# Performance work log

Measured on AMD Instinct MI355X. Metric: run time of the kernel, lower is better.

## Reference

```python
import jax, jax.numpy as jnp
import numpy as np

N = 102400      # total nodes across batch of graphs
E = 1638400     # edges (before self-loops)
G = 256         # number of graphs
F_IN = 64       # node_feat_dim
H = 4           # heads (conv1)
C = 32          # hidden per head
CLIN = 5
NEG_SLOPE = 0.2


def setup_inputs() -> dict:
    key = jax.random.key(0)
    ks = jax.random.split(key, 16)
    s = 0.1
    x = jax.random.normal(ks[0], (N, F_IN), jnp.float32)
    edge_index = jax.random.randint(ks[1], (2, E), 0, N, dtype=jnp.int32)
    batch = (jnp.arange(N, dtype=jnp.int32) * G) // N  # sorted graph ids, 400 nodes each
    clinical = jax.random.normal(ks[2], (G, CLIN), jnp.float32)
    W1 = jax.random.normal(ks[3], (F_IN, H * C), jnp.float32) * s
    a_src1 = jax.random.normal(ks[4], (H, C), jnp.float32) * s
    a_dst1 = jax.random.normal(ks[5], (H, C), jnp.float32) * s
    b1 = jnp.zeros((H * C,), jnp.float32)
    # GATConv 2: 128 -> 32, 1 head, no concat (mean over heads = identity for 1 head)
    W2 = jax.random.normal(ks[6], (H * C, C), jnp.float32) * s
    a_src2 = jax.random.normal(ks[7], (1, C), jnp.float32) * s
    a_dst2 = jax.random.normal(ks[8], (1, C), jnp.float32) * s
    b2 = jnp.zeros((C,), jnp.float32)
    # Classifier: Linear(37,16) -> ELU -> Linear(16,1)
    Wc1 = jax.random.normal(ks[9], (C + CLIN, 16), jnp.float32) * s
    bc1 = jnp.zeros((16,), jnp.float32)
    Wc2 = jax.random.normal(ks[10], (16, 1), jnp.float32) * s
    bc2 = jnp.zeros((1,), jnp.float32)
    return dict(x=x, edge_index=edge_index, batch=batch, clinical=clinical,
                W1=W1, a_src1=a_src1, a_dst1=a_dst1, b1=b1,
                W2=W2, a_src2=a_src2, a_dst2=a_dst2, b2=b2,
                Wc1=Wc1, bc1=bc1, Wc2=Wc2, bc2=bc2)


def _gat(x, W, a_src, a_dst, b, src, dst, heads, concat):
    n = x.shape[0]
    h = (x @ W).reshape(n, heads, -1)                 # [N, H, C]
    al_src = jnp.einsum('nhc,hc->nh', h, a_src)       # [N, H]
    al_dst = jnp.einsum('nhc,hc->nh', h, a_dst)
    e = jax.nn.leaky_relu(al_src[src] + al_dst[dst], NEG_SLOPE)  # [E, H]
    # segment softmax over incoming edges of each destination node
    m = jax.ops.segment_max(e, dst, num_segments=n)
    ex = jnp.exp(e - m[dst])
    den = jax.ops.segment_sum(ex, dst, num_segments=n)
    alpha = ex / den[dst]                             # [E, H]
    msg = h[src] * alpha[:, :, None]                  # [E, H, C]
    out = jax.ops.segment_sum(msg, dst, num_segments=n)
    out = out.reshape(n, -1) if concat else out.mean(axis=1)
    return out + b


def reference(x, edge_index, batch, clinical,
              W1, a_src1, a_dst1, b1, W2, a_src2, a_dst2, b2,
              Wc1, bc1, Wc2, bc2):
    n = x.shape[0]
    loop = jnp.arange(n, dtype=edge_index.dtype)
    src = jnp.concatenate([edge_index[0], loop])      # PyG add_self_loops=True
    dst = jnp.concatenate([edge_index[1], loop])
    h = _gat(x, W1, a_src1, a_dst1, b1, src, dst, H, True)   # [N, 128]
    h = jax.nn.elu(h)
    h = _gat(h, W2, a_src2, a_dst2, b2, src, dst, 1, False)  # [N, 32]
    h = jax.nn.elu(h)
    # global mean pool per graph
    sums = jax.ops.segment_sum(h, batch, num_segments=G)
    cnt = jax.ops.segment_sum(jnp.ones((n,), h.dtype), batch, num_segments=G)
    pooled = sums / cnt[:, None]                      # [G, 32]
    fused = jnp.concatenate([pooled, clinical.reshape(-1, CLIN)], axis=1)  # [G, 37]
    z = jax.nn.elu(fused @ Wc1 + bc1)
    return z @ Wc2 + bc2                              # [G, 1]
```

## Files before the change

kernel.cpp:

```cpp
#include <hip/hip_runtime.h>
#include <math.h>

#define N_NODES 102400
#define N_EDGES 1638400
#define G_GRAPHS 256
#define NODES_PER_G 400
#define CAPB 7168
#define F_IN  64
#define H1    4
#define C1    32
#define F_MID 128
#define C2    32
#define CLIN  5
#define NEG   0.2f

__device__ __forceinline__ float lrelu(float x) { return x > 0.f ? x : NEG * x; }
__device__ __forceinline__ float elu(float x)   { return x > 0.f ? x : expm1f(x); }

__device__ __forceinline__ unsigned short f2bf(float f) {
    unsigned u = __float_as_uint(f);
    u = (u + 0x7fffu + ((u >> 16) & 1u)) >> 16;
    return (unsigned short)u;
}
__device__ __forceinline__ float bfLO(unsigned p) { return __uint_as_float(p << 16); }
__device__ __forceinline__ float bfHI(unsigned p) { return __uint_as_float(p & 0xffff0000u); }
__device__ __forceinline__ float4 bf2f4(uint2 p) {
    return make_float4(__uint_as_float(p.x << 16), __uint_as_float(p.x & 0xffff0000u),
                       __uint_as_float(p.y << 16), __uint_as_float(p.y & 0xffff0000u));
}

__global__ __launch_bounds__(256) void bin_k(const int* __restrict__ ei,
                                             int* __restrict__ gcnt,
                                             unsigned* __restrict__ binned) {
    __shared__ int hist[256];
    __shared__ int off[256];
    int t = threadIdx.x;
    hist[t] = 0;
    __syncthreads();
    int i0 = blockIdx.x * 4096;
#pragma unroll
    for (int j = 0; j < 16; ++j) {
        int d = ei[N_EDGES + i0 + j * 256 + t];
        atomicAdd(&hist[d / NODES_PER_G], 1);
    }
    __syncthreads();
    off[t] = atomicAdd(&gcnt[t], hist[t]);
    hist[t] = 0;
    __syncthreads();
#pragma unroll
    for (int j = 0; j < 16; ++j) {
        int idx = i0 + j * 256 + t;
        int s = ei[idx];
        int d = ei[N_EDGES + idx];
        int g = d / NODES_PER_G;
        int dl = d - g * NODES_PER_G;
        int slot = atomicAdd(&hist[g], 1);
        binned[(size_t)g * CAPB + off[g] + slot] = (unsigned)s | ((unsigned)dl << 17);
    }
}

__global__ __launch_bounds__(512) void build_k(
    const int* __restrict__ gcnt, unsigned* __restrict__ binned,
    int* __restrict__ row_ptr, int* __restrict__ row_end)
{
    __shared__ unsigned edg[CAPB];
    __shared__ int coll[CAPB];
    __shared__ int hist[512];
    __shared__ int cur[NODES_PER_G];
    int g = blockIdx.x, t = threadIdx.x;
    int ne = gcnt[g];
    size_t base = (size_t)g * CAPB;
    for (int i = t; i < ne; i += 512) edg[i] = binned[base + i];
    hist[t] = 0;
    __syncthreads();
    for (int i = t; i < ne; i += 512) atomicAdd(&hist[edg[i] >> 17], 1);
    __syncthreads();
    int v = hist[t];
    for (int off = 1; off < 512; off <<= 1) {
        int tmp = (t >= off) ? hist[t - off] : 0;
        __syncthreads();
        hist[t] += tmp;
        __syncthreads();
    }
    int excl = hist[t] - v;
    if (t < NODES_PER_G) {
        cur[t] = excl;
        row_ptr[g * NODES_PER_G + t] = (int)base + excl;
    }
    __syncthreads();
    for (int i = t; i < ne; i += 512) {
        unsigned e = edg[i];
        int pos = atomicAdd(&cur[e >> 17], 1);
        coll[pos] = (int)(e & 0x1FFFFu);
    }
    __syncthreads();
    if (t < NODES_PER_G) row_end[g * NODES_PER_G + t] = (int)base + cur[t];
    for (int i = t; i < ne; i += 512) binned[base + i] = (unsigned)coll[i];
}

__global__ __launch_bounds__(256) void ht_k(
    const float* __restrict__ x, const float* __restrict__ W1,
    const float* __restrict__ a_src1, const float* __restrict__ a_dst1,
    unsigned short* __restrict__ hth, float* __restrict__ al1)
{
    __shared__ float xs[32][65];
    __shared__ float W1s[64 * 160];
    int t = threadIdx.x;
    int n0 = blockIdx.x * 32;
#pragma unroll
    for (int j = 0; j < 8; ++j) {
        int idx = t + 256 * j;
        xs[idx >> 6][idx & 63] = x[(size_t)n0 * F_IN + idx];
    }
#pragma unroll
    for (int j = 0; j < 8; ++j) {
        int q = t + 256 * j;
        int k = q >> 5, c0 = (q & 31) * 4;
        float4 v = ((const float4*)W1)[q];
        *(float4*)&W1s[k * 160 + (c0 >> 4) * 20 + (c0 & 15)] = v;
    }
    __syncthreads();
    int n = t >> 3, cg = t & 7;
    float acc[16];
#pragma unroll
    for (int j = 0; j < 16; ++j) acc[j] = 0.f;
    const float* wp = &W1s[cg * 20];
#pragma unroll 4
    for (int k = 0; k < F_IN; ++k) {
        float a = xs[n][k];
        const float* wr = wp + k * 160;
#pragma unroll
        for (int j = 0; j < 4; ++j) {
            float4 w = *(const float4*)(wr + 4 * j);
            acc[4 * j + 0] += a * w.x;
            acc[4 * j + 1] += a * w.y;
            acc[4 * j + 2] += a * w.z;
            acc[4 * j + 3] += a * w.w;
        }
    }
    int head = cg >> 1, hoff = (cg & 1) * 16;
    const float* asp = a_src1 + head * 32 + hoff;
    const float* adp = a_dst1 + head * 32 + hoff;
    float ps = 0.f, pd = 0.f;
#pragma unroll
    for (int j = 0; j < 16; ++j) { ps += acc[j] * asp[j]; pd += acc[j] * adp[j]; }
    ps += __shfl_xor(ps, 1);
    pd += __shfl_xor(pd, 1);
    if ((cg & 1) == 0) {
        al1[(size_t)(n0 + n) * 8 + head]     = ps;
        al1[(size_t)(n0 + n) * 8 + 4 + head] = pd;
    }
    unsigned u[8];
#pragma unroll
    for (int j = 0; j < 8; ++j)
        u[j] = ((unsigned)f2bf(acc[2 * j + 1]) << 16) | (unsigned)f2bf(acc[2 * j]);
    uint4* hp = (uint4*)(hth + ((size_t)(n0 + n) * F_MID + cg * 16));
    hp[0] = make_uint4(u[0], u[1], u[2], u[3]);
    hp[1] = make_uint4(u[4], u[5], u[6], u[7]);
}

__global__ __launch_bounds__(256, 8) void agg1_k(
    const int* __restrict__ row_ptr, const int* __restrict__ row_end,
    const unsigned* __restrict__ col, const unsigned short* __restrict__ hth,
    const float* __restrict__ al1, const float* __restrict__ b1,
    float* __restrict__ h1)
{
    int t = threadIdx.x;
    int wv = t >> 6, lane = t & 63, h = lane >> 4;
    int d = blockIdx.x * 4 + wv;
    const unsigned* hv = (const unsigned*)hth;

    float adv = al1[d * 8 + 4 + h];
    float w = __expf(lrelu(al1[d * 8 + h] + adv));
    unsigned p = hv[(size_t)d * 64 + lane];
    float a0 = w * bfLO(p), a1 = w * bfHI(p);
    float den = w;

    int e0 = __builtin_amdgcn_readfirstlane(row_ptr[d]);
    int e1 = __builtin_amdgcn_readfirstlane(row_end[d]);
    int e = e0;
    for (; e + 8 <= e1; e += 8) {
        int s0 = __builtin_amdgcn_readfirstlane((int)col[e]);
        int s1 = __builtin_amdgcn_readfirstlane((int)col[e + 1]);
        int s2 = __builtin_amdgcn_readfirstlane((int)col[e + 2]);
        int s3 = __builtin_amdgcn_readfirstlane((int)col[e + 3]);
        int s4 = __builtin_amdgcn_readfirstlane((int)col[e + 4]);
        int s5 = __builtin_amdgcn_readfirstlane((int)col[e + 5]);
        int s6 = __builtin_amdgcn_readfirstlane((int)col[e + 6]);
        int s7 = __builtin_amdgcn_readfirstlane((int)col[e + 7]);
        unsigned p0 = hv[(size_t)s0 * 64 + lane];
        unsigned p1 = hv[(size_t)s1 * 64 + lane];
        unsigned p2 = hv[(size_t)s2 * 64 + lane];
        unsigned p3 = hv[(size_t)s3 * 64 + lane];
        unsigned p4 = hv[(size_t)s4 * 64 + lane];
        unsigned p5 = hv[(size_t)s5 * 64 + lane];
        unsigned p6 = hv[(size_t)s6 * 64 + lane];
        unsigned p7 = hv[(size_t)s7 * 64 + lane];
        float v0 = al1[s0 * 8 + h];
        float v1 = al1[s1 * 8 + h];
        float v2 = al1[s2 * 8 + h];
        float v3 = al1[s3 * 8 + h];
        float v4 = al1[s4 * 8 + h];
        float v5 = al1[s5 * 8 + h];
        float v6 = al1[s6 * 8 + h];
        float v7 = al1[s7 * 8 + h];
        float w0 = __expf(lrelu(v0 + adv));
        float w1 = __expf(lrelu(v1 + adv));
        float w2 = __expf(lrelu(v2 + adv));
        float w3 = __expf(lrelu(v3 + adv));
        float w4 = __expf(lrelu(v4 + adv));
        float w5 = __expf(lrelu(v5 + adv));
        float w6 = __expf(lrelu(v6 + adv));
        float w7 = __expf(lrelu(v7 + adv));
        a0 += w0 * bfLO(p0) + w1 * bfLO(p1) + w2 * bfLO(p2) + w3 * bfLO(p3);
        a0 += w4 * bfLO(p4) + w5 * bfLO(p5) + w6 * bfLO(p6) + w7 * bfLO(p7);
        a1 += w0 * bfHI(p0) + w1 * bfHI(p1) + w2 * bfHI(p2) + w3 * bfHI(p3);
        a1 += w4 * bfHI(p4) + w5 * bfHI(p5) + w6 * bfHI(p6) + w7 * bfHI(p7);
        den += w0 + w1 + w2 + w3 + w4 + w5 + w6 + w7;
    }
    for (; e < e1; ++e) {
        int s = __builtin_amdgcn_readfirstlane((int)col[e]);
        unsigned ps_ = hv[(size_t)s * 64 + lane];
        float av = al1[s * 8 + h];
        float we = __expf(lrelu(av + adv));
        a0 += we * bfLO(ps_);
        a1 += we * bfHI(ps_);
        den += we;
    }
    float inv = 1.f / den;
    float2 bb = ((const float2*)b1)[lane];
    float2 o;
    o.x = elu(a0 * inv + bb.x);
    o.y = elu(a1 * inv + bb.y);
    ((float2*)h1)[(size_t)d * 64 + lane] = o;
}

__global__ __launch_bounds__(256) void dense2_k(
    const float* __restrict__ h1, const float* __restrict__ W2,
    const float* __restrict__ a_src2, const float* __restrict__ a_dst2,
    unsigned short* __restrict__ h2h, float* __restrict__ al_s2, float* __restrict__ al_d2)
{
    __shared__ float hs[32 * 132];
    __shared__ float W2s[128 * 32];
    __shared__ float h2s[32 * 36];
    int t = threadIdx.x;
    int n0 = blockIdx.x * 32;
#pragma unroll
    for (int j = 0; j < 4; ++j) {
        int q = t + 256 * j;
        int n = q >> 5, c0 = (q & 31) * 4;
        *(float4*)&hs[n * 132 + c0] = ((const float4*)h1)[(size_t)n0 * 32 + q];
        ((float4*)W2s)[q] = ((const float4*)W2)[q];
    }
    __syncthreads();
    int n = t >> 3, o4 = (t & 7) * 4;
    float4 acc = make_float4(0.f, 0.f, 0.f, 0.f);
#pragma unroll 8
    for (int k = 0; k < F_MID; ++k) {
        float a = hs[n * 132 + k];
        float4 w = *(const float4*)&W2s[k * 32 + o4];
        acc.x += a * w.x; acc.y += a * w.y; acc.z += a * w.z; acc.w += a * w.w;
    }
    unsigned lo = ((unsigned)f2bf(acc.y) << 16) | (unsigned)f2bf(acc.x);
    unsigned hi = ((unsigned)f2bf(acc.w) << 16) | (unsigned)f2bf(acc.z);
    ((uint2*)h2h)[(((size_t)(n0 + n)) * C2 + o4) >> 2] = make_uint2(lo, hi);
    *(float4*)&h2s[n * 36 + o4] = acc;
    __syncthreads();
    if (t < 64) {
        int which = t >> 5, nn = t & 31;
        const float* a = which ? a_dst2 : a_src2;
        float s = 0.f;
#pragma unroll
        for (int k = 0; k < C2; ++k) s += h2s[nn * 36 + k] * a[k];
        if (which) al_d2[n0 + nn] = s;
        else       al_s2[n0 + nn] = s;
    }
}

__global__ __launch_bounds__(256) void gather2(
    const int* __restrict__ row_ptr, const int* __restrict__ row_end,
    const unsigned* __restrict__ col, const float* __restrict__ al_src,
    const float* __restrict__ al_dst, const unsigned short* __restrict__ h2h,
    const float* __restrict__ b2, const int* __restrict__ batch,
    float* __restrict__ pooled)
{
    __shared__ float sv[32][C2];
    int t = threadIdx.x;
    int r = t >> 3;
    int c = t & 7;
    int d = blockIdx.x * 32 + r;
    const uint2* h2v = (const uint2*)h2h;
    float ad = al_dst[d];
    float w = __expf(lrelu(al_src[d] + ad));
    float4 v = bf2f4(h2v[(size_t)d * 8 + c]);
    float ax = w * v.x, ay = w * v.y, az = w * v.z, aw = w * v.w;
    float den = w;
    int e0 = row_ptr[d], e1 = row_end[d];
    int e = e0;
    for (; e + 4 <= e1; e += 4) {
        int s0 = (int)col[e], s1 = (int)col[e + 1], s2 = (int)col[e + 2], s3 = (int)col[e + 3];
        uint2 p0 = h2v[(size_t)s0 * 8 + c];
        uint2 p1 = h2v[(size_t)s1 * 8 + c];
        uint2 p2 = h2v[(size_t)s2 * 8 + c];
        uint2 p3 = h2v[(size_t)s3 * 8 + c];
        float4 v0 = bf2f4(p0);
        float4 v1 = bf2f4(p1);
        float4 v2 = bf2f4(p2);
        float4 v3 = bf2f4(p3);
        float w0 = __expf(lrelu(al_src[s0] + ad));
        float w1 = __expf(lrelu(al_src[s1] + ad));
        float w2 = __expf(lrelu(al_src[s2] + ad));
        float w3 = __expf(lrelu(al_src[s3] + ad));
        ax += w0 * v0.x + w1 * v1.x + w2 * v2.x + w3 * v3.x;
        ay += w0 * v0.y + w1 * v1.y + w2 * v2.y + w3 * v3.y;
        az += w0 * v0.z + w1 * v1.z + w2 * v2.z + w3 * v3.z;
        aw += w0 * v0.w + w1 * v1.w + w2 * v2.w + w3 * v3.w;
        den += w0 + w1 + w2 + w3;
    }
    for (; e < e1; ++e) {
        int s = (int)col[e];
        float4 vs = bf2f4(h2v[(size_t)s * 8 + c]);
        float we = __expf(lrelu(al_src[s] + ad));
        ax += we * vs.x; ay += we * vs.y; az += we * vs.z; aw += we * vs.w;
        den += we;
    }
    float inv = 1.f / den;
    const float4 bv = ((const float4*)b2)[c];
    sv[r][4 * c + 0] = elu(ax * inv + bv.x);
    sv[r][4 * c + 1] = elu(ay * inv + bv.y);
    sv[r][4 * c + 2] = elu(az * inv + bv.z);
    sv[r][4 * c + 3] = elu(aw * inv + bv.w);
    __syncthreads();
    int d0 = blockIdx.x * 32;
    int g0 = batch[d0], g1 = batch[d0 + 31];
    if (t < 64) {
        int which = t >> 5, ch = t & 31;
        int g = which ? g1 : g0;
        if (which == 0 || g1 != g0) {
            float s = 0.f;
            for (int rr = 0; rr < 32; ++rr)
                if (batch[d0 + rr] == g) s += sv[rr][ch];
            atomicAdd(&pooled[g * C2 + ch], s);
        }
    }
}

__global__ __launch_bounds__(256) void head_k(
    const float* __restrict__ pooled, const float* __restrict__ clinical,
    const float* __restrict__ Wc1, const float* __restrict__ bc1,
    const float* __restrict__ Wc2, const float* __restrict__ bc2,
    float* __restrict__ out)
{
    int g = threadIdx.x;
    float fused[C2 + CLIN];
    const float inv = 1.f / 400.f;
#pragma unroll
    for (int c = 0; c < C2; ++c) fused[c] = pooled[g * C2 + c] * inv;
#pragma unroll
    for (int c = 0; c < CLIN; ++c) fused[C2 + c] = clinical[g * CLIN + c];
    float o = bc2[0];
#pragma unroll
    for (int j = 0; j < 16; ++j) {
        float acc = bc1[j];
#pragma unroll
        for (int k = 0; k < C2 + CLIN; ++k) acc += fused[k] * Wc1[k * 16 + j];
        o += (acc > 0.f ? acc : expm1f(acc)) * Wc2[j];
    }
    out[g] = o;
}

extern "C" void kernel_launch(void* const* d_in, const int* in_sizes, int n_in,
                              void* d_out, int out_size, void* d_ws, size_t ws_size,
                              hipStream_t stream) {
    const float* x        = (const float*)d_in[0];
    const int*   ei       = (const int*)  d_in[1];
    const int*   batch    = (const int*)  d_in[2];
    const float* clinical = (const float*)d_in[3];
    const float* W1       = (const float*)d_in[4];
    const float* a_src1   = (const float*)d_in[5];
    const float* a_dst1   = (const float*)d_in[6];
    const float* b1       = (const float*)d_in[7];
    const float* W2       = (const float*)d_in[8];
    const float* a_src2   = (const float*)d_in[9];
    const float* a_dst2   = (const float*)d_in[10];
    const float* b2       = (const float*)d_in[11];
    const float* Wc1      = (const float*)d_in[12];
    const float* bc1      = (const float*)d_in[13];
    const float* Wc2      = (const float*)d_in[14];
    const float* bc2      = (const float*)d_in[15];
    float* out = (float*)d_out;

    const size_t N = N_NODES;
    float* ws = (float*)d_ws;
    size_t off = 0;
    float* al1    = ws + off; off += N * 8;
    float* al_s2  = ws + off; off += N;
    float* al_d2  = ws + off; off += N;
    float* pooled = ws + off; off += (size_t)G_GRAPHS * C2;
    unsigned short* hth = (unsigned short*)(ws + off); off += N * F_MID / 2;
    float* h1     = ws + off; off += N * F_MID;
    unsigned short* h2h = (unsigned short*)(ws + off); off += N * C2 / 2;
    int* row_ptr = (int*)(ws + off); off += N;
    int* row_end = (int*)(ws + off); off += N;
    int* gcnt    = (int*)(ws + off); off += 256;
    unsigned* binned = (unsigned*)(ws + off); off += (size_t)G_GRAPHS * CAPB;

    hipMemsetAsync(gcnt, 0, 256 * sizeof(int), stream);
    hipMemsetAsync(pooled, 0, G_GRAPHS * C2 * sizeof(float), stream);

    bin_k  <<<N_EDGES / 4096, 256, 0, stream>>>(ei, gcnt, binned);
    build_k<<<G_GRAPHS, 512, 0, stream>>>(gcnt, binned, row_ptr, row_end);

    ht_k<<<N_NODES / 32, 256, 0, stream>>>(x, W1, a_src1, a_dst1, hth, al1);

    agg1_k<<<N_NODES / 4, 256, 0, stream>>>(row_ptr, row_end, binned, hth, al1, b1, h1);

    dense2_k<<<N_NODES / 32, 256, 0, stream>>>(h1, W2, a_src2, a_dst2, h2h, al_s2, al_d2);

    gather2<<<N_NODES / 32, 256, 0, stream>>>(row_ptr, row_end, binned, al_s2, al_d2, h2h,
                                              b2, batch, pooled);

    head_k<<<1, G_GRAPHS, 0, stream>>>(pooled, clinical, Wc1, bc1, Wc2, bc2, out);
}
```

Baseline: 318.3 us.

## Fuse layer-2 dense projection into layer-1 aggregation and split attention arrays

Folds the dense2 kernel (h1 @ W2 plus layer-2 attention logits) into the layer-1 aggregation kernel. Each wave keeps its aggregated row in shared memory and multiplies it by a shared-memory copy of W2, so the 128-wide fp32 h1 tensor is never written to or read from global memory. Blocks grow to 1024 threads, and the source/destination attention logits are split into separate arrays to tighten the gather. Scalar edge tails become one masked, batched step in both aggregation kernels. The larger blocks and the extra 16KB W2 tile per block may limit occupancy in the gather-heavy kernel.

```diff
diff --git a/kernel.cpp b/kernel.cpp
--- a/kernel.cpp
+++ b/kernel.cpp
@@ -101,7 +101,7 @@
 __global__ __launch_bounds__(256) void ht_k(
     const float* __restrict__ x, const float* __restrict__ W1,
     const float* __restrict__ a_src1, const float* __restrict__ a_dst1,
-    unsigned short* __restrict__ hth, float* __restrict__ al1)
+    unsigned short* __restrict__ hth, float* __restrict__ als1, float* __restrict__ ald1)
 {
     __shared__ float xs[32][65];
     __shared__ float W1s[64 * 160];
@@ -147,8 +147,8 @@
     ps += __shfl_xor(ps, 1);
     pd += __shfl_xor(pd, 1);
     if ((cg & 1) == 0) {
-        al1[(size_t)(n0 + n) * 8 + head]     = ps;
-        al1[(size_t)(n0 + n) * 8 + 4 + head] = pd;
+        als1[(size_t)(n0 + n) * 4 + head] = ps;
+        ald1[(size_t)(n0 + n) * 4 + head] = pd;
     }
     unsigned u[8];
 #pragma unroll
@@ -159,19 +159,29 @@
     hp[1] = make_uint4(u[4], u[5], u[6], u[7]);
 }
 
-__global__ __launch_bounds__(256, 8) void agg1_k(
+__global__ __launch_bounds__(1024, 8) void agg1_k(
     const int* __restrict__ row_ptr, const int* __restrict__ row_end,
     const unsigned* __restrict__ col, const unsigned short* __restrict__ hth,
-    const float* __restrict__ al1, const float* __restrict__ b1,
-    float* __restrict__ h1)
+    const float* __restrict__ als1, const float* __restrict__ ald1,
+    const float* __restrict__ b1, const float* __restrict__ W2,
+    const float* __restrict__ a_src2, const float* __restrict__ a_dst2,
+    unsigned short* __restrict__ h2h, float* __restrict__ al_s2, float* __restrict__ al_d2)
 {
+    __shared__ float W2s[128 * 32];
+    __shared__ float a2s[64];
+    __shared__ float h1L[16 * 128];
+
     int t = threadIdx.x;
+    ((float4*)W2s)[t] = ((const float4*)W2)[t];
+    if (t < 32) { a2s[t] = a_src2[t]; a2s[32 + t] = a_dst2[t]; }
+    __syncthreads();
+
     int wv = t >> 6, lane = t & 63, h = lane >> 4;
-    int d = blockIdx.x * 4 + wv;
+    int d = blockIdx.x * 16 + wv;
     const unsigned* hv = (const unsigned*)hth;
 
-    float adv = al1[d * 8 + 4 + h];
-    float w = __expf(lrelu(al1[d * 8 + h] + adv));
+    float adv = ald1[d * 4 + h];
+    float w = __expf(lrelu(als1[d * 4 + h] + adv));
     unsigned p = hv[(size_t)d * 64 + lane];
     float a0 = w * bfLO(p), a1 = w * bfHI(p);
     float den = w;
@@ -196,14 +206,14 @@
         unsigned p5 = hv[(size_t)s5 * 64 + lane];
         unsigned p6 = hv[(size_t)s6 * 64 + lane];
         unsigned p7 = hv[(size_t)s7 * 64 + lane];
-        float v0 = al1[s0 * 8 + h];
-        float v1 = al1[s1 * 8 + h];
-        float v2 = al1[s2 * 8 + h];
-        float v3 = al1[s3 * 8 + h];
-        float v4 = al1[s4 * 8 + h];
-        float v5 = al1[s5 * 8 + h];
-        float v6 = al1[s6 * 8 + h];
-        float v7 = al1[s7 * 8 + h];
+        float v0 = als1[s0 * 4 + h];
+        float v1 = als1[s1 * 4 + h];
+        float v2 = als1[s2 * 4 + h];
+        float v3 = als1[s3 * 4 + h];
+        float v4 = als1[s4 * 4 + h];
+        float v5 = als1[s5 * 4 + h];
+        float v6 = als1[s6 * 4 + h];
+        float v7 = als1[s7 * 4 + h];
         float w0 = __expf(lrelu(v0 + adv));
         float w1 = __expf(lrelu(v1 + adv));
         float w2 = __expf(lrelu(v2 + adv));
@@ -218,62 +228,75 @@
         a1 += w4 * bfHI(p4) + w5 * bfHI(p5) + w6 * bfHI(p6) + w7 * bfHI(p7);
         den += w0 + w1 + w2 + w3 + w4 + w5 + w6 + w7;
     }
-    for (; e < e1; ++e) {
-        int s = __builtin_amdgcn_readfirstlane((int)col[e]);
-        unsigned ps_ = hv[(size_t)s * 64 + lane];
-        float av = al1[s * 8 + h];
-        float we = __expf(lrelu(av + adv));
-        a0 += we * bfLO(ps_);
-        a1 += we * bfHI(ps_);
-        den += we;
+    if (e < e1) {
+        int last = e1 - 1;
+        int i1 = (e + 1 < e1) ? e + 1 : last;
+        int i2 = (e + 2 < e1) ? e + 2 : last;
+        int i3 = (e + 3 < e1) ? e + 3 : last;
+        int i4 = (e + 4 < e1) ? e + 4 : last;
+        int i5 = (e + 5 < e1) ? e + 5 : last;
+        int i6 = (e + 6 < e1) ? e + 6 : last;
+        int i7 = (e + 7 < e1) ? e + 7 : last;
+        int s0 = __builtin_amdgcn_readfirstlane((int)col[e]);
+        int s1 = __builtin_amdgcn_readfirstlane((int)col[i1]);
+        int s2 = __builtin_amdgcn_readfirstlane((int)col[i2]);
+        int s3 = __builtin_amdgcn_readfirstlane((int)col[i3]);
+        int s4 = __builtin_amdgcn_readfirstlane((int)col[i4]);
+        int s5 = __builtin_amdgcn_readfirstlane((int)col[i5]);
+        int s6 = __builtin_amdgcn_readfirstlane((int)col[i6]);
+        int s7 = __builtin_amdgcn_readfirstlane((int)col[i7]);
+        unsigned p0 = hv[(size_t)s0 * 64 + lane];
+        unsigned p1 = hv[(size_t)s1 * 64 + lane];
+        unsigned p2 = hv[(size_t)s2 * 64 + lane];
+        unsigned p3 = hv[(size_t)s3 * 64 + lane];
+        unsigned p4 = hv[(size_t)s4 * 64 + lane];
+        unsigned p5 = hv[(size_t)s5 * 64 + lane];
+        unsigned p6 = hv[(size_t)s6 * 64 + lane];
+        unsigned p7 = hv[(size_t)s7 * 64 + lane];
+        float w0 = __expf(lrelu(als1[s0 * 4 + h] + adv));
+        float w1 = (e + 1 < e1) ? __expf(lrelu(als1[s1 * 4 + h] + adv)) : 0.f;
+        float w2 = (e + 2 < e1) ? __expf(lrelu(als1[s2 * 4 + h] + adv)) : 0.f;
+        float w3 = (e + 3 < e1) ? __expf(lrelu(als1[s3 * 4 + h] + adv)) : 0.f;
+        float w4 = (e + 4 < e1) ? __expf(lrelu(als1[s4 * 4 + h] + adv)) : 0.f;
+        float w5 = (e + 5 < e1) ? __expf(lrelu(als1[s5 * 4 + h] + adv)) : 0.f;
+        float w6 = (e + 6 < e1) ? __expf(lrelu(als1[s6 * 4 + h] + adv)) : 0.f;
+        float w7 = (e + 7 < e1) ? __expf(lrelu(als1[s7 * 4 + h] + adv)) : 0.f;
+        a0 += w0 * bfLO(p0) + w1 * bfLO(p1) + w2 * bfLO(p2) + w3 * bfLO(p3);
+        a0 += w4 * bfLO(p4) + w5 * bfLO(p5) + w6 * bfLO(p6) + w7 * bfLO(p7);
+        a1 += w0 * bfHI(p0) + w1 * bfHI(p1) + w2 * bfHI(p2) + w3 * bfHI(p3);
+        a1 += w4 * bfHI(p4) + w5 * bfHI(p5) + w6 * bfHI(p6) + w7 * bfHI(p7);
+        den += w0 + w1 + w2 + w3 + w4 + w5 + w6 + w7;
     }
     float inv = 1.f / den;
     float2 bb = ((const float2*)b1)[lane];
-    float2 o;
-    o.x = elu(a0 * inv + bb.x);
-    o.y = elu(a1 * inv + bb.y);
-    ((float2*)h1)[(size_t)d * 64 + lane] = o;
-}
-
-__global__ __launch_bounds__(256) void dense2_k(
-    const float* __restrict__ h1, const float* __restrict__ W2,
-    const float* __restrict__ a_src2, const float* __restrict__ a_dst2,
-    unsigned short* __restrict__ h2h, float* __restrict__ al_s2, float* __restrict__ al_d2)
-{
-    __shared__ float hs[32 * 132];
-    __shared__ float W2s[128 * 32];
-    __shared__ float h2s[32 * 36];
-    int t = threadIdx.x;
-    int n0 = blockIdx.x * 32;
-#pragma unroll
-    for (int j = 0; j < 4; ++j) {
-        int q = t + 256 * j;
-        int n = q >> 5, c0 = (q & 31) * 4;
-        *(float4*)&hs[n * 132 + c0] = ((const float4*)h1)[(size_t)n0 * 32 + q];
-        ((float4*)W2s)[q] = ((const float4*)W2)[q];
-    }
-    __syncthreads();
-    int n = t >> 3, o4 = (t & 7) * 4;
-    float4 acc = make_float4(0.f, 0.f, 0.f, 0.f);
-#pragma unroll 8
-    for (int k = 0; k < F_MID; ++k) {
-        float a = hs[n * 132 + k];
-        float4 w = *(const float4*)&W2s[k * 32 + o4];
-        acc.x += a * w.x; acc.y += a * w.y; acc.z += a * w.z; acc.w += a * w.w;
-    }
-    unsigned lo = ((unsigned)f2bf(acc.y) << 16) | (unsigned)f2bf(acc.x);
-    unsigned hi = ((unsigned)f2bf(acc.w) << 16) | (unsigned)f2bf(acc.z);
-    ((uint2*)h2h)[(((size_t)(n0 + n)) * C2 + o4) >> 2] = make_uint2(lo, hi);
-    *(float4*)&h2s[n * 36 + o4] = acc;
-    __syncthreads();
-    if (t < 64) {
-        int which = t >> 5, nn = t & 31;
-        const float* a = which ? a_dst2 : a_src2;
-        float s = 0.f;
-#pragma unroll
-        for (int k = 0; k < C2; ++k) s += h2s[nn * 36 + k] * a[k];
-        if (which) al_d2[n0 + nn] = s;
-        else       al_s2[n0 + nn] = s;
+    float h1a = elu(a0 * inv + bb.x);
+    float h1b = elu(a1 * inv + bb.y);
+
+    h1L[wv * 128 + 2 * lane]     = h1a;
+    h1L[wv * 128 + 2 * lane + 1] = h1b;
+    int o = lane & 31, kh = lane >> 5;
+    const float* hp = &h1L[wv * 128 + kh * 64];
+    const float* wp2 = &W2s[kh * 64 * 32 + o];
+    float v = 0.f;
+#pragma unroll 16
+    for (int k = 0; k < 64; ++k) v += hp[k] * wp2[k * 32];
+    v += __shfl_xor(v, 32);
+
+    float coef = a2s[kh * 32 + o];
+    float pl = v * coef;
+    pl += __shfl_xor(pl, 1);
+    pl += __shfl_xor(pl, 2);
+    pl += __shfl_xor(pl, 4);
+    pl += __shfl_xor(pl, 8);
+    pl += __shfl_xor(pl, 16);
+    if (o == 0) {
+        if (kh == 0) al_s2[d] = pl;
+        else         al_d2[d] = pl;
+    }
+    float vn = __shfl_xor(v, 1);
+    if (kh == 0 && (o & 1) == 0) {
+        unsigned u = ((unsigned)f2bf(vn) << 16) | (unsigned)f2bf(v);
+        ((unsigned*)h2h)[(size_t)d * 16 + (o >> 1)] = u;
     }
 }
 
@@ -317,12 +340,25 @@
         aw += w0 * v0.w + w1 * v1.w + w2 * v2.w + w3 * v3.w;
         den += w0 + w1 + w2 + w3;
     }
-    for (; e < e1; ++e) {
-        int s = (int)col[e];
-        float4 vs = bf2f4(h2v[(size_t)s * 8 + c]);
-        float we = __expf(lrelu(al_src[s] + ad));
-        ax += we * vs.x; ay += we * vs.y; az += we * vs.z; aw += we * vs.w;
-        den += we;
+    if (e < e1) {
+        int last = e1 - 1;
+        int i1 = (e + 1 < e1) ? e + 1 : last;
+        int i2 = (e + 2 < e1) ? e + 2 : last;
+        int s0 = (int)col[e], s1 = (int)col[i1], s2 = (int)col[i2];
+        uint2 p0 = h2v[(size_t)s0 * 8 + c];
+        uint2 p1 = h2v[(size_t)s1 * 8 + c];
+        uint2 p2 = h2v[(size_t)s2 * 8 + c];
+        float4 v0 = bf2f4(p0);
+        float4 v1 = bf2f4(p1);
+        float4 v2 = bf2f4(p2);
+        float w0 = __expf(lrelu(al_src[s0] + ad));
+        float w1 = (e + 1 < e1) ? __expf(lrelu(al_src[s1] + ad)) : 0.f;
+        float w2 = (e + 2 < e1) ? __expf(lrelu(al_src[s2] + ad)) : 0.f;
+        ax += w0 * v0.x + w1 * v1.x + w2 * v2.x;
+        ay += w0 * v0.y + w1 * v1.y + w2 * v2.y;
+        az += w0 * v0.z + w1 * v1.z + w2 * v2.z;
+        aw += w0 * v0.w + w1 * v1.w + w2 * v2.w;
+        den += w0 + w1 + w2;
     }
     float inv = 1.f / den;
     const float4 bv = ((const float4*)b2)[c];
@@ -393,12 +429,12 @@
     const size_t N = N_NODES;
     float* ws = (float*)d_ws;
     size_t off = 0;
-    float* al1    = ws + off; off += N * 8;
+    float* als1   = ws + off; off += N * 4;
+    float* ald1   = ws + off; off += N * 4;
     float* al_s2  = ws + off; off += N;
     float* al_d2  = ws + off; off += N;
     float* pooled = ws + off; off += (size_t)G_GRAPHS * C2;
     unsigned short* hth = (unsigned short*)(ws + off); off += N * F_MID / 2;
-    float* h1     = ws + off; off += N * F_MID;
     unsigned short* h2h = (unsigned short*)(ws + off); off += N * C2 / 2;
     int* row_ptr = (int*)(ws + off); off += N;
     int* row_end = (int*)(ws + off); off += N;
@@ -411,11 +447,10 @@
     bin_k  <<<N_EDGES / 4096, 256, 0, stream>>>(ei, gcnt, binned);
     build_k<<<G_GRAPHS, 512, 0, stream>>>(gcnt, binned, row_ptr, row_end);
 
-    ht_k<<<N_NODES / 32, 256, 0, stream>>>(x, W1, a_src1, a_dst1, hth, al1);
-
-    agg1_k<<<N_NODES / 4, 256, 0, stream>>>(row_ptr, row_end, binned, hth, al1, b1, h1);
-
-    dense2_k<<<N_NODES / 32, 256, 0, stream>>>(h1, W2, a_src2, a_dst2, h2h, al_s2, al_d2);
+    ht_k<<<N_NODES / 32, 256, 0, stream>>>(x, W1, a_src1, a_dst1, hth, als1, ald1);
+
+    agg1_k<<<N_NODES / 16, 1024, 0, stream>>>(row_ptr, row_end, binned, hth, als1, ald1,
+                                              b1, W2, a_src2, a_dst2, h2h, al_s2, al_d2);
 
     gather2<<<N_NODES / 32, 256, 0, stream>>>(row_ptr, row_end, binned, al_s2, al_d2, h2h,
                                               b2, batch, pooled);
```

Result: faster. 305.8 us (-3.9%).

## Restructure layer-2 gather to wave-per-node with edge-parallel lanes; split logits

Applied to the files above, without the earlier changes.

Layer-2 aggregation now assigns a full wave per destination node, with four lane groups each handling different edges and 16 lanes covering channel pairs. Partial sums are combined by cross-lane shuffles and each 4-node block issues one pooled atomic. Layer-1 source/destination attention logits are stored in separate compact arrays, and the agg1 remainder loop becomes a single masked 8-wide batch. The aim is more memory-level parallelism in the gathers and less tail serialization, at the cost of more blocks and more atomics on the pooled buffer.

```diff
diff --git a/kernel.cpp b/kernel.cpp
--- a/kernel.cpp
+++ b/kernel.cpp
@@ -24,10 +24,6 @@
 }
 __device__ __forceinline__ float bfLO(unsigned p) { return __uint_as_float(p << 16); }
 __device__ __forceinline__ float bfHI(unsigned p) { return __uint_as_float(p & 0xffff0000u); }
-__device__ __forceinline__ float4 bf2f4(uint2 p) {
-    return make_float4(__uint_as_float(p.x << 16), __uint_as_float(p.x & 0xffff0000u),
-                       __uint_as_float(p.y << 16), __uint_as_float(p.y & 0xffff0000u));
-}
 
 __global__ __launch_bounds__(256) void bin_k(const int* __restrict__ ei,
                                              int* __restrict__ gcnt,
@@ -101,7 +97,7 @@
 __global__ __launch_bounds__(256) void ht_k(
     const float* __restrict__ x, const float* __restrict__ W1,
     const float* __restrict__ a_src1, const float* __restrict__ a_dst1,
-    unsigned short* __restrict__ hth, float* __restrict__ al1)
+    unsigned short* __restrict__ hth, float* __restrict__ als1, float* __restrict__ ald1)
 {
     __shared__ float xs[32][65];
     __shared__ float W1s[64 * 160];
@@ -147,8 +143,8 @@
     ps += __shfl_xor(ps, 1);
     pd += __shfl_xor(pd, 1);
     if ((cg & 1) == 0) {
-        al1[(size_t)(n0 + n) * 8 + head]     = ps;
-        al1[(size_t)(n0 + n) * 8 + 4 + head] = pd;
+        als1[(size_t)(n0 + n) * 4 + head] = ps;
+        ald1[(size_t)(n0 + n) * 4 + head] = pd;
     }
     unsigned u[8];
 #pragma unroll
@@ -162,16 +158,16 @@
 __global__ __launch_bounds__(256, 8) void agg1_k(
     const int* __restrict__ row_ptr, const int* __restrict__ row_end,
     const unsigned* __restrict__ col, const unsigned short* __restrict__ hth,
-    const float* __restrict__ al1, const float* __restrict__ b1,
-    float* __restrict__ h1)
+    const float* __restrict__ als1, const float* __restrict__ ald1,
+    const float* __restrict__ b1, float* __restrict__ h1)
 {
     int t = threadIdx.x;
     int wv = t >> 6, lane = t & 63, h = lane >> 4;
     int d = blockIdx.x * 4 + wv;
     const unsigned* hv = (const unsigned*)hth;
 
-    float adv = al1[d * 8 + 4 + h];
-    float w = __expf(lrelu(al1[d * 8 + h] + adv));
+    float adv = ald1[d * 4 + h];
+    float w = __expf(lrelu(als1[d * 4 + h] + adv));
     unsigned p = hv[(size_t)d * 64 + lane];
     float a0 = w * bfLO(p), a1 = w * bfHI(p);
     float den = w;
@@ -196,14 +192,14 @@
         unsigned p5 = hv[(size_t)s5 * 64 + lane];
         unsigned p6 = hv[(size_t)s6 * 64 + lane];
         unsigned p7 = hv[(size_t)s7 * 64 + lane];
-        float v0 = al1[s0 * 8 + h];
-        float v1 = al1[s1 * 8 + h];
-        float v2 = al1[s2 * 8 + h];
-        float v3 = al1[s3 * 8 + h];
-        float v4 = al1[s4 * 8 + h];
-        float v5 = al1[s5 * 8 + h];
-        float v6 = al1[s6 * 8 + h];
-        float v7 = al1[s7 * 8 + h];
+        float v0 = als1[s0 * 4 + h];
+        float v1 = als1[s1 * 4 + h];
+        float v2 = als1[s2 * 4 + h];
+        float v3 = als1[s3 * 4 + h];
+        float v4 = als1[s4 * 4 + h];
+        float v5 = als1[s5 * 4 + h];
+        float v6 = als1[s6 * 4 + h];
+        float v7 = als1[s7 * 4 + h];
         float w0 = __expf(lrelu(v0 + adv));
         float w1 = __expf(lrelu(v1 + adv));
         float w2 = __expf(lrelu(v2 + adv));
@@ -218,14 +214,44 @@
         a1 += w4 * bfHI(p4) + w5 * bfHI(p5) + w6 * bfHI(p6) + w7 * bfHI(p7);
         den += w0 + w1 + w2 + w3 + w4 + w5 + w6 + w7;
     }
-    for (; e < e1; ++e) {
-        int s = __builtin_amdgcn_readfirstlane((int)col[e]);
-        unsigned ps_ = hv[(size_t)s * 64 + lane];
-        float av = al1[s * 8 + h];
-        float we = __expf(lrelu(av + adv));
-        a0 += we * bfLO(ps_);
-        a1 += we * bfHI(ps_);
-        den += we;
+    if (e < e1) {
+        int last = e1 - 1;
+        int i1 = (e + 1 < e1) ? e + 1 : last;
+        int i2 = (e + 2 < e1) ? e + 2 : last;
+        int i3 = (e + 3 < e1) ? e + 3 : last;
+        int i4 = (e + 4 < e1) ? e + 4 : last;
+        int i5 = (e + 5 < e1) ? e + 5 : last;
+        int i6 = (e + 6 < e1) ? e + 6 : last;
+        int i7 = (e + 7 < e1) ? e + 7 : last;
+        int s0 = __builtin_amdgcn_readfirstlane((int)col[e]);
+        int s1 = __builtin_amdgcn_readfirstlane((int)col[i1]);
+        int s2 = __builtin_amdgcn_readfirstlane((int)col[i2]);
+        int s3 = __builtin_amdgcn_readfirstlane((int)col[i3]);
+        int s4 = __builtin_amdgcn_readfirstlane((int)col[i4]);
+        int s5 = __builtin_amdgcn_readfirstlane((int)col[i5]);
+        int s6 = __builtin_amdgcn_readfirstlane((int)col[i6]);
+        int s7 = __builtin_amdgcn_readfirstlane((int)col[i7]);
+        unsigned p0 = hv[(size_t)s0 * 64 + lane];
+        unsigned p1 = hv[(size_t)s1 * 64 + lane];
+        unsigned p2 = hv[(size_t)s2 * 64 + lane];
+        unsigned p3 = hv[(size_t)s3 * 64 + lane];
+        unsigned p4 = hv[(size_t)s4 * 64 + lane];
+        unsigned p5 = hv[(size_t)s5 * 64 + lane];
+        unsigned p6 = hv[(size_t)s6 * 64 + lane];
+        unsigned p7 = hv[(size_t)s7 * 64 + lane];
+        float w0 = __expf(lrelu(als1[s0 * 4 + h] + adv));
+        float w1 = (e + 1 < e1) ? __expf(lrelu(als1[s1 * 4 + h] + adv)) : 0.f;
+        float w2 = (e + 2 < e1) ? __expf(lrelu(als1[s2 * 4 + h] + adv)) : 0.f;
+        float w3 = (e + 3 < e1) ? __expf(lrelu(als1[s3 * 4 + h] + adv)) : 0.f;
+        float w4 = (e + 4 < e1) ? __expf(lrelu(als1[s4 * 4 + h] + adv)) : 0.f;
+        float w5 = (e + 5 < e1) ? __expf(lrelu(als1[s5 * 4 + h] + adv)) : 0.f;
+        float w6 = (e + 6 < e1) ? __expf(lrelu(als1[s6 * 4 + h] + adv)) : 0.f;
+        float w7 = (e + 7 < e1) ? __expf(lrelu(als1[s7 * 4 + h] + adv)) : 0.f;
+        a0 += w0 * bfLO(p0) + w1 * bfLO(p1) + w2 * bfLO(p2) + w3 * bfLO(p3);
+        a0 += w4 * bfLO(p4) + w5 * bfLO(p5) + w6 * bfLO(p6) + w7 * bfLO(p7);
+        a1 += w0 * bfHI(p0) + w1 * bfHI(p1) + w2 * bfHI(p2) + w3 * bfHI(p3);
+        a1 += w4 * bfHI(p4) + w5 * bfHI(p5) + w6 * bfHI(p6) + w7 * bfHI(p7);
+        den += w0 + w1 + w2 + w3 + w4 + w5 + w6 + w7;
     }
     float inv = 1.f / den;
     float2 bb = ((const float2*)b1)[lane];
@@ -277,71 +303,69 @@
     }
 }
 
-__global__ __launch_bounds__(256) void gather2(
+__global__ __launch_bounds__(256, 8) void gather2(
     const int* __restrict__ row_ptr, const int* __restrict__ row_end,
     const unsigned* __restrict__ col, const float* __restrict__ al_src,
     const float* __restrict__ al_dst, const unsigned short* __restrict__ h2h,
     const float* __restrict__ b2, const int* __restrict__ batch,
     float* __restrict__ pooled)
 {
-    __shared__ float sv[32][C2];
+    __shared__ float sm[4][C2];
     int t = threadIdx.x;
-    int r = t >> 3;
-    int c = t & 7;
-    int d = blockIdx.x * 32 + r;
-    const uint2* h2v = (const uint2*)h2h;
+    int wv = t >> 6, lane = t & 63;
+    int q = lane >> 4, cp = lane & 15;
+    int d = blockIdx.x * 4 + wv;
+    const unsigned* hv = (const unsigned*)h2h;
+
     float ad = al_dst[d];
-    float w = __expf(lrelu(al_src[d] + ad));
-    float4 v = bf2f4(h2v[(size_t)d * 8 + c]);
-    float ax = w * v.x, ay = w * v.y, az = w * v.z, aw = w * v.w;
-    float den = w;
-    int e0 = row_ptr[d], e1 = row_end[d];
+    float a0 = 0.f, a1 = 0.f, den = 0.f;
+    if (q == 0) {
+        float ws = __expf(lrelu(al_src[d] + ad));
+        unsigned p = hv[(size_t)d * 16 + cp];
+        a0 = ws * bfLO(p); a1 = ws * bfHI(p); den = ws;
+    }
+    int e0 = __builtin_amdgcn_readfirstlane(row_ptr[d]);
+    int e1 = __builtin_amdgcn_readfirstlane(row_end[d]);
     int e = e0;
-    for (; e + 4 <= e1; e += 4) {
-        int s0 = (int)col[e], s1 = (int)col[e + 1], s2 = (int)col[e + 2], s3 = (int)col[e + 3];
-        uint2 p0 = h2v[(size_t)s0 * 8 + c];
-        uint2 p1 = h2v[(size_t)s1 * 8 + c];
-        uint2 p2 = h2v[(size_t)s2 * 8 + c];
-        uint2 p3 = h2v[(size_t)s3 * 8 + c];
-        float4 v0 = bf2f4(p0);
-        float4 v1 = bf2f4(p1);
-        float4 v2 = bf2f4(p2);
-        float4 v3 = bf2f4(p3);
-        float w0 = __expf(lrelu(al_src[s0] + ad));
-        float w1 = __expf(lrelu(al_src[s1] + ad));
-        float w2 = __expf(lrelu(al_src[s2] + ad));
-        float w3 = __expf(lrelu(al_src[s3] + ad));
-        ax += w0 * v0.x + w1 * v1.x + w2 * v2.x + w3 * v3.x;
-        ay += w0 * v0.y + w1 * v1.y + w2 * v2.y + w3 * v3.y;
-        az += w0 * v0.z + w1 * v1.z + w2 * v2.z + w3 * v3.z;
-        aw += w0 * v0.w + w1 * v1.w + w2 * v2.w + w3 * v3.w;
-        den += w0 + w1 + w2 + w3;
-    }
-    for (; e < e1; ++e) {
-        int s = (int)col[e];
-        float4 vs = bf2f4(h2v[(size_t)s * 8 + c]);
-        float we = __expf(lrelu(al_src[s] + ad));
-        ax += we * vs.x; ay += we * vs.y; az += we * vs.z; aw += we * vs.w;
-        den += we;
-    }
-    float inv = 1.f / den;
-    const float4 bv = ((const float4*)b2)[c];
-    sv[r][4 * c + 0] = elu(ax * inv + bv.x);
-    sv[r][4 * c + 1] = elu(ay * inv + bv.y);
-    sv[r][4 * c + 2] = elu(az * inv + bv.z);
-    sv[r][4 * c + 3] = elu(aw * inv + bv.w);
-    __syncthreads();
-    int d0 = blockIdx.x * 32;
-    int g0 = batch[d0], g1 = batch[d0 + 31];
-    if (t < 64) {
-        int which = t >> 5, ch = t & 31;
-        int g = which ? g1 : g0;
-        if (which == 0 || g1 != g0) {
-            float s = 0.f;
-            for (int rr = 0; rr < 32; ++rr)
-                if (batch[d0 + rr] == g) s += sv[rr][ch];
-            atomicAdd(&pooled[g * C2 + ch], s);
-        }
+    for (; e + 8 <= e1; e += 8) {
+        int sa = (int)col[e + q];
+        int sb = (int)col[e + 4 + q];
+        unsigned pa = hv[(size_t)sa * 16 + cp];
+        unsigned pb = hv[(size_t)sb * 16 + cp];
+        float wa = __expf(lrelu(al_src[sa] + ad));
+        float wb = __expf(lrelu(al_src[sb] + ad));
+        a0 += wa * bfLO(pa) + wb * bfLO(pb);
+        a1 += wa * bfHI(pa) + wb * bfHI(pb);
+        den += wa + wb;
+    }
+    if (e < e1) {
+        int last = e1 - 1;
+        int ia = e + q;     bool ma = ia < e1; ia = ma ? ia : last;
+        int ib = e + 4 + q; bool mb = ib < e1; ib = mb ? ib : last;
+        int sa = (int)col[ia];
+        int sb = (int)col[ib];
+        unsigned pa = hv[(size_t)sa * 16 + cp];
+        unsigned pb = hv[(size_t)sb * 16 + cp];
+        float wa = ma ? __expf(lrelu(al_src[sa] + ad)) : 0.f;
+        float wb = mb ? __expf(lrelu(al_src[sb] + ad)) : 0.f;
+        a0 += wa * bfLO(pa) + wb * bfLO(pb);
+        a1 += wa * bfHI(pa) + wb * bfHI(pb);
+        den += wa + wb;
+    }
+    a0 += __shfl_xor(a0, 16);  a0 += __shfl_xor(a0, 32);
+    a1 += __shfl_xor(a1, 16);  a1 += __shfl_xor(a1, 32);
+    den += __shfl_xor(den, 16); den += __shfl_xor(den, 32);
+    if (q == 0) {
+        float inv = 1.f / den;
+        float2 bb = ((const float2*)b2)[cp];
+        sm[wv][2 * cp]     = elu(a0 * inv + bb.x);
+        sm[wv][2 * cp + 1] = elu(a1 * inv + bb.y);
+    }
+    __syncthreads();
+    if (t < C2) {
+        float s = sm[0][t] + sm[1][t] + sm[2][t] + sm[3][t];
+        int g = batch[blockIdx.x * 4];
+        atomicAdd(&pooled[g * C2 + t], s);
     }
 }
 
@@ -393,7 +417,8 @@
     const size_t N = N_NODES;
     float* ws = (float*)d_ws;
     size_t off = 0;
-    float* al1    = ws + off; off += N * 8;
+    float* als1   = ws + off; off += N * 4;
+    float* ald1   = ws + off; off += N * 4;
     float* al_s2  = ws + off; off += N;
     float* al_d2  = ws + off; off += N;
     float* pooled = ws + off; off += (size_t)G_GRAPHS * C2;
@@ -411,14 +436,15 @@
     bin_k  <<<N_EDGES / 4096, 256, 0, stream>>>(ei, gcnt, binned);
     build_k<<<G_GRAPHS, 512, 0, stream>>>(gcnt, binned, row_ptr, row_end);
 
-    ht_k<<<N_NODES / 32, 256, 0, stream>>>(x, W1, a_src1, a_dst1, hth, al1);
-
-    agg1_k<<<N_NODES / 4, 256, 0, stream>>>(row_ptr, row_end, binned, hth, al1, b1, h1);
+    ht_k<<<N_NODES / 32, 256, 0, stream>>>(x, W1, a_src1, a_dst1, hth, als1, ald1);
+
+    agg1_k<<<N_NODES / 4, 256, 0, stream>>>(row_ptr, row_end, binned, hth, als1, ald1,
+                                            b1, h1);
 
     dense2_k<<<N_NODES / 32, 256, 0, stream>>>(h1, W2, a_src2, a_dst2, h2h, al_s2, al_d2);
 
-    gather2<<<N_NODES / 32, 256, 0, stream>>>(row_ptr, row_end, binned, al_s2, al_d2, h2h,
-                                              b2, batch, pooled);
+    gather2<<<N_NODES / 4, 256, 0, stream>>>(row_ptr, row_end, binned, al_s2, al_d2, h2h,
+                                             b2, batch, pooled);
 
     head_k<<<1, G_GRAPHS, 0, stream>>>(pooled, clinical, Wc1, bc1, Wc2, bc2, out);
 }
```

Result: slower. 341.3 us (+7.2%).

## Compute edge attention weights once per lane and broadcast via shuffles in agg1

Applied to the files above, without the earlier changes.

Splits the per-node layer-1 attention scalars into separate src and dst arrays of 4 floats. In agg1, each batch of 8 edges is loaded with one vector load and broadcast via readlane. Each of 32 lanes computes one (edge, head) exp weight, and the weights are shared across the wave with shuffles, so lanes no longer each compute 8 redundant exps and gathers. The scalar tail loops in both aggregation kernels become a single predicated, padded batch. The cost is extra cross-lane shuffle traffic, and the padded tail batch issues redundant loads.

```diff
diff --git a/kernel.cpp b/kernel.cpp
--- a/kernel.cpp
+++ b/kernel.cpp
@@ -101,7 +101,7 @@
 __global__ __launch_bounds__(256) void ht_k(
     const float* __restrict__ x, const float* __restrict__ W1,
     const float* __restrict__ a_src1, const float* __restrict__ a_dst1,
-    unsigned short* __restrict__ hth, float* __restrict__ al1)
+    unsigned short* __restrict__ hth, float* __restrict__ als1, float* __restrict__ ald1)
 {
     __shared__ float xs[32][65];
     __shared__ float W1s[64 * 160];
@@ -147,8 +147,8 @@
     ps += __shfl_xor(ps, 1);
     pd += __shfl_xor(pd, 1);
     if ((cg & 1) == 0) {
-        al1[(size_t)(n0 + n) * 8 + head]     = ps;
-        al1[(size_t)(n0 + n) * 8 + 4 + head] = pd;
+        als1[(size_t)(n0 + n) * 4 + head] = ps;
+        ald1[(size_t)(n0 + n) * 4 + head] = pd;
     }
     unsigned u[8];
 #pragma unroll
@@ -162,32 +162,38 @@
 __global__ __launch_bounds__(256, 8) void agg1_k(
     const int* __restrict__ row_ptr, const int* __restrict__ row_end,
     const unsigned* __restrict__ col, const unsigned short* __restrict__ hth,
-    const float* __restrict__ al1, const float* __restrict__ b1,
-    float* __restrict__ h1)
+    const float* __restrict__ als1, const float* __restrict__ ald1,
+    const float* __restrict__ b1, float* __restrict__ h1)
 {
     int t = threadIdx.x;
     int wv = t >> 6, lane = t & 63, h = lane >> 4;
+    int hw = (lane >> 3) & 3;
+    int ew = lane & 7;
     int d = blockIdx.x * 4 + wv;
     const unsigned* hv = (const unsigned*)hth;
 
-    float adv = al1[d * 8 + 4 + h];
-    float w = __expf(lrelu(al1[d * 8 + h] + adv));
+    float adv  = ald1[d * 4 + h];
+    float advB = ald1[d * 4 + hw];
+    float w = __expf(lrelu(als1[d * 4 + h] + adv));
     unsigned p = hv[(size_t)d * 64 + lane];
     float a0 = w * bfLO(p), a1 = w * bfHI(p);
     float den = w;
+
+    int bidx = (h << 3);
 
     int e0 = __builtin_amdgcn_readfirstlane(row_ptr[d]);
     int e1 = __builtin_amdgcn_readfirstlane(row_end[d]);
     int e = e0;
     for (; e + 8 <= e1; e += 8) {
-        int s0 = __builtin_amdgcn_readfirstlane((int)col[e]);
-        int s1 = __builtin_amdgcn_readfirstlane((int)col[e + 1]);
-        int s2 = __builtin_amdgcn_readfirstlane((int)col[e + 2]);
-        int s3 = __builtin_amdgcn_readfirstlane((int)col[e + 3]);
-        int s4 = __builtin_amdgcn_readfirstlane((int)col[e + 4]);
-        int s5 = __builtin_amdgcn_readfirstlane((int)col[e + 5]);
-        int s6 = __builtin_amdgcn_readfirstlane((int)col[e + 6]);
-        int s7 = __builtin_amdgcn_readfirstlane((int)col[e + 7]);
+        unsigned sv = col[e + ew];
+        int s0 = __builtin_amdgcn_readlane(sv, 0);
+        int s1 = __builtin_amdgcn_readlane(sv, 1);
+        int s2 = __builtin_amdgcn_readlane(sv, 2);
+        int s3 = __builtin_amdgcn_readlane(sv, 3);
+        int s4 = __builtin_amdgcn_readlane(sv, 4);
+        int s5 = __builtin_amdgcn_readlane(sv, 5);
+        int s6 = __builtin_amdgcn_readlane(sv, 6);
+        int s7 = __builtin_amdgcn_readlane(sv, 7);
         unsigned p0 = hv[(size_t)s0 * 64 + lane];
         unsigned p1 = hv[(size_t)s1 * 64 + lane];
         unsigned p2 = hv[(size_t)s2 * 64 + lane];
@@ -196,36 +202,57 @@
         unsigned p5 = hv[(size_t)s5 * 64 + lane];
         unsigned p6 = hv[(size_t)s6 * 64 + lane];
         unsigned p7 = hv[(size_t)s7 * 64 + lane];
-        float v0 = al1[s0 * 8 + h];
-        float v1 = al1[s1 * 8 + h];
-        float v2 = al1[s2 * 8 + h];
-        float v3 = al1[s3 * 8 + h];
-        float v4 = al1[s4 * 8 + h];
-        float v5 = al1[s5 * 8 + h];
-        float v6 = al1[s6 * 8 + h];
-        float v7 = al1[s7 * 8 + h];
-        float w0 = __expf(lrelu(v0 + adv));
-        float w1 = __expf(lrelu(v1 + adv));
-        float w2 = __expf(lrelu(v2 + adv));
-        float w3 = __expf(lrelu(v3 + adv));
-        float w4 = __expf(lrelu(v4 + adv));
-        float w5 = __expf(lrelu(v5 + adv));
-        float w6 = __expf(lrelu(v6 + adv));
-        float w7 = __expf(lrelu(v7 + adv));
+        float avv  = als1[(size_t)sv * 4 + hw];
+        float wAll = __expf(lrelu(avv + advB));
+        float w0 = __shfl(wAll, bidx + 0);
+        float w1 = __shfl(wAll, bidx + 1);
+        float w2 = __shfl(wAll, bidx + 2);
+        float w3 = __shfl(wAll, bidx + 3);
+        float w4 = __shfl(wAll, bidx + 4);
+        float w5 = __shfl(wAll, bidx + 5);
+        float w6 = __shfl(wAll, bidx + 6);
+        float w7 = __shfl(wAll, bidx + 7);
         a0 += w0 * bfLO(p0) + w1 * bfLO(p1) + w2 * bfLO(p2) + w3 * bfLO(p3);
         a0 += w4 * bfLO(p4) + w5 * bfLO(p5) + w6 * bfLO(p6) + w7 * bfLO(p7);
         a1 += w0 * bfHI(p0) + w1 * bfHI(p1) + w2 * bfHI(p2) + w3 * bfHI(p3);
         a1 += w4 * bfHI(p4) + w5 * bfHI(p5) + w6 * bfHI(p6) + w7 * bfHI(p7);
         den += w0 + w1 + w2 + w3 + w4 + w5 + w6 + w7;
     }
-    for (; e < e1; ++e) {
-        int s = __builtin_amdgcn_readfirstlane((int)col[e]);
-        unsigned ps_ = hv[(size_t)s * 64 + lane];
-        float av = al1[s * 8 + h];
-        float we = __expf(lrelu(av + adv));
-        a0 += we * bfLO(ps_);
-        a1 += we * bfHI(ps_);
-        den += we;
+    if (e < e1) {
+        int iv = e + ew;
+        bool inr = iv < e1;
+        unsigned sv = col[inr ? iv : (e1 - 1)];
+        int s0 = __builtin_amdgcn_readlane(sv, 0);
+        int s1 = __builtin_amdgcn_readlane(sv, 1);
+        int s2 = __builtin_amdgcn_readlane(sv, 2);
+        int s3 = __builtin_amdgcn_readlane(sv, 3);
+        int s4 = __builtin_amdgcn_readlane(sv, 4);
+        int s5 = __builtin_amdgcn_readlane(sv, 5);
+        int s6 = __builtin_amdgcn_readlane(sv, 6);
+        int s7 = __builtin_amdgcn_readlane(sv, 7);
+        unsigned p0 = hv[(size_t)s0 * 64 + lane];
+        unsigned p1 = hv[(size_t)s1 * 64 + lane];
+        unsigned p2 = hv[(size_t)s2 * 64 + lane];
+        unsigned p3 = hv[(size_t)s3 * 64 + lane];
+        unsigned p4 = hv[(size_t)s4 * 64 + lane];
+        unsigned p5 = hv[(size_t)s5 * 64 + lane];
+        unsigned p6 = hv[(size_t)s6 * 64 + lane];
+        unsigned p7 = hv[(size_t)s7 * 64 + lane];
+        float avv  = als1[(size_t)sv * 4 + hw];
+        float wAll = inr ? __expf(lrelu(avv + advB)) : 0.f;
+        float w0 = __shfl(wAll, bidx + 0);
+        float w1 = __shfl(wAll, bidx + 1);
+        float w2 = __shfl(wAll, bidx + 2);
+        float w3 = __shfl(wAll, bidx + 3);
+        float w4 = __shfl(wAll, bidx + 4);
+        float w5 = __shfl(wAll, bidx + 5);
+        float w6 = __shfl(wAll, bidx + 6);
+        float w7 = __shfl(wAll, bidx + 7);
+        a0 += w0 * bfLO(p0) + w1 * bfLO(p1) + w2 * bfLO(p2) + w3 * bfLO(p3);
+        a0 += w4 * bfLO(p4) + w5 * bfLO(p5) + w6 * bfLO(p6) + w7 * bfLO(p7);
+        a1 += w0 * bfHI(p0) + w1 * bfHI(p1) + w2 * bfHI(p2) + w3 * bfHI(p3);
+        a1 += w4 * bfHI(p4) + w5 * bfHI(p5) + w6 * bfHI(p6) + w7 * bfHI(p7);
+        den += w0 + w1 + w2 + w3 + w4 + w5 + w6 + w7;
     }
     float inv = 1.f / den;
     float2 bb = ((const float2*)b1)[lane];
@@ -317,12 +344,25 @@
         aw += w0 * v0.w + w1 * v1.w + w2 * v2.w + w3 * v3.w;
         den += w0 + w1 + w2 + w3;
     }
-    for (; e < e1; ++e) {
-        int s = (int)col[e];
-        float4 vs = bf2f4(h2v[(size_t)s * 8 + c]);
-        float we = __expf(lrelu(al_src[s] + ad));
-        ax += we * vs.x; ay += we * vs.y; az += we * vs.z; aw += we * vs.w;
-        den += we;
+    if (e < e1) {
+        int last = e1 - 1;
+        int i1 = (e + 1 < e1) ? e + 1 : last;
+        int i2 = (e + 2 < e1) ? e + 2 : last;
+        int s0 = (int)col[e], s1 = (int)col[i1], s2 = (int)col[i2];
+        uint2 p0 = h2v[(size_t)s0 * 8 + c];
+        uint2 p1 = h2v[(size_t)s1 * 8 + c];
+        uint2 p2 = h2v[(size_t)s2 * 8 + c];
+        float4 v0 = bf2f4(p0);
+        float4 v1 = bf2f4(p1);
+        float4 v2 = bf2f4(p2);
+        float w0 = __expf(lrelu(al_src[s0] + ad));
+        float w1 = (e + 1 < e1) ? __expf(lrelu(al_src[s1] + ad)) : 0.f;
+        float w2 = (e + 2 < e1) ? __expf(lrelu(al_src[s2] + ad)) : 0.f;
+        ax += w0 * v0.x + w1 * v1.x + w2 * v2.x;
+        ay += w0 * v0.y + w1 * v1.y + w2 * v2.y;
+        az += w0 * v0.z + w1 * v1.z + w2 * v2.z;
+        aw += w0 * v0.w + w1 * v1.w + w2 * v2.w;
+        den += w0 + w1 + w2;
     }
     float inv = 1.f / den;
     const float4 bv = ((const float4*)b2)[c];
@@ -393,7 +433,8 @@
     const size_t N = N_NODES;
     float* ws = (float*)d_ws;
     size_t off = 0;
-    float* al1    = ws + off; off += N * 8;
+    float* als1   = ws + off; off += N * 4;
+    float* ald1   = ws + off; off += N * 4;
     float* al_s2  = ws + off; off += N;
     float* al_d2  = ws + off; off += N;
     float* pooled = ws + off; off += (size_t)G_GRAPHS * C2;
@@ -411,9 +452,10 @@
     bin_k  <<<N_EDGES / 4096, 256, 0, stream>>>(ei, gcnt, binned);
     build_k<<<G_GRAPHS, 512, 0, stream>>>(gcnt, binned, row_ptr, row_end);
 
-    ht_k<<<N_NODES / 32, 256, 0, stream>>>(x, W1, a_src1, a_dst1, hth, al1);
-
-    agg1_k<<<N_NODES / 4, 256, 0, stream>>>(row_ptr, row_end, binned, hth, al1, b1, h1);
+    ht_k<<<N_NODES / 32, 256, 0, stream>>>(x, W1, a_src1, a_dst1, hth, als1, ald1);
+
+    agg1_k<<<N_NODES / 4, 256, 0, stream>>>(row_ptr, row_end, binned, hth, als1, ald1,
+                                            b1, h1);
 
     dense2_k<<<N_NODES / 32, 256, 0, stream>>>(h1, W2, a_src2, a_dst2, h2h, al_s2, al_d2);
 
```

Measured after the change: 310.0 us. 1.03x faster.
